# Kernel tuning notes

Hardware: AMD Instinct MI355X
Metric: run time of the kernel (lower is better)

## Reference

```python
import jax, jax.numpy as jnp
import numpy as np

HEADS = 16
DIM_HEAD = 64
EPS = 1e-12  # F.normalize default eps


def setup_inputs() -> dict:
    key = jax.random.key(0)
    k1, k2, k3 = jax.random.split(key, 3)
    b, n, dim = 2, 2048, 1024
    dim_inner = HEADS * DIM_HEAD
    x = jax.random.normal(k1, (b, n, dim), dtype=jnp.float32)
    gamma = jnp.ones((dim,), dtype=jnp.float32)
    w_qkv = jax.random.normal(k2, (dim, 3 * dim_inner), dtype=jnp.float32) * 0.02
    w_out = jax.random.normal(k3, (dim_inner, dim), dtype=jnp.float32) * 0.02
    return {"x": x, "gamma": gamma, "w_qkv": w_qkv, "w_out": w_out}


def reference(x, gamma, w_qkv, w_out):
    b, n, dim = x.shape
    h, d = HEADS, DIM_HEAD
    scale = d ** -0.5

    # RMSNorm (lucidrains): F.normalize(x, dim=-1) * dim**0.5 * gamma
    norm = jnp.sqrt(jnp.sum(x * x, axis=-1, keepdims=True))
    xn = x / jnp.maximum(norm, EPS) * (dim ** 0.5) * gamma

    # qkv projection -> [b, n, 3, h, d] -> q/k/v each [b, h, n, d]
    qkv = (xn @ w_qkv).reshape(b, n, 3, h, d)
    qkv = jnp.transpose(qkv, (2, 0, 3, 1, 4))
    q, k, v = qkv[0], qkv[1], qkv[2]

    q = q * scale
    sim = jnp.einsum('bhid,bhjd->bhij', q, k)  # [b, h, n, n]
    causal_mask = jnp.triu(jnp.ones((n, n), dtype=bool), k=1)
    mask_value = -jnp.finfo(sim.dtype).max
    sim = jnp.where(causal_mask, mask_value, sim)
    attn = jax.nn.softmax(sim, axis=-1)
    out = jnp.einsum('bhij,bhjd->bhid', attn, v)  # [b, h, n, d]

    out = jnp.transpose(out, (0, 2, 1, 3)).reshape(b, n, h * d)
    return out @ w_out
```

## Files before the change

### kernel.cpp

```cpp
#include <hip/hip_runtime.h>

typedef __attribute__((ext_vector_type(8))) short bf16x8;
typedef __attribute__((ext_vector_type(4))) short bf16x4;
typedef __attribute__((ext_vector_type(4))) float f32x4;

static __device__ __forceinline__ short f2bf(float f) {
    union { float f; unsigned u; } v; v.f = f;
    unsigned r = v.u + 0x7fffu + ((v.u >> 16) & 1u);
    return (short)(r >> 16);
}

static __device__ __forceinline__ void async_copy16(const short* g, short* l) {
    __builtin_amdgcn_global_load_lds((const __attribute__((address_space(1))) void*)g,
                                     (__attribute__((address_space(3))) void*)l,
                                     16, 0, 0);
}

#define HEADS 16
#define DHEAD 64
#define NSEQ  2048
#define DIM   1024
#define BATCH 2
#define ROWS  (BATCH * NSEQ)
#define NQKV  (3 * HEADS * DHEAD)

__global__ __launch_bounds__(256) void prep_kernel(const float* __restrict__ x,
                                                   const float* __restrict__ gamma,
                                                   const float* __restrict__ w_qkv,
                                                   const float* __restrict__ w_out,
                                                   short* __restrict__ xn,
                                                   short* __restrict__ wqkvT,
                                                   short* __restrict__ woutT) {
    const int blk = blockIdx.x;
    const int t = threadIdx.x;
    __shared__ float tile[64][65];
    __shared__ float part[4];

    if (blk < 1024) {
        const float* in;  short* out;  int C, bx, by;
        if (blk < 768) { in = w_qkv; out = wqkvT; C = NQKV; bx = blk % 48; by = blk / 48; }
        else           { in = w_out; out = woutT; C = DIM;  bx = (blk - 768) & 15; by = (blk - 768) >> 4; }
        const int gx = bx * 64, gy = by * 64;
        const int lc4 = (t & 15) * 4;
        const int lr  = t >> 4;
#pragma unroll
        for (int p = 0; p < 4; ++p) {
            const float4 v = *(const float4*)&in[(size_t)(gy + p * 16 + lr) * C + gx + lc4];
            tile[p * 16 + lr][lc4 + 0] = v.x;
            tile[p * 16 + lr][lc4 + 1] = v.y;
            tile[p * 16 + lr][lc4 + 2] = v.z;
            tile[p * 16 + lr][lc4 + 3] = v.w;
        }
        __syncthreads();
        const int oc  = t >> 2;
        const int or4 = (t & 3) * 16;
#pragma unroll
        for (int j = 0; j < 4; ++j) {
            bf16x4 w;
#pragma unroll
            for (int r = 0; r < 4; ++r) w[r] = f2bf(tile[or4 + j * 4 + r][oc]);
            *(bf16x4*)&out[(size_t)(gx + oc) * DIM + gy + or4 + j * 4] = w;
        }
    } else {
        const int row = blk - 1024;
        const float4 v = ((const float4*)(x + (size_t)row * DIM))[t];
        float s = v.x * v.x + v.y * v.y + v.z * v.z + v.w * v.w;
#pragma unroll
        for (int off = 32; off > 0; off >>= 1) s += __shfl_down(s, off, 64);
        if ((t & 63) == 0) part[t >> 6] = s;
        __syncthreads();
        const float tot = part[0] + part[1] + part[2] + part[3];
        const float scale = 32.0f / fmaxf(sqrtf(tot), 1e-12f);
        const float4 g = ((const float4*)gamma)[t];
        bf16x4 o;
        o[0] = f2bf(v.x * scale * g.x);
        o[1] = f2bf(v.y * scale * g.y);
        o[2] = f2bf(v.z * scale * g.z);
        o[3] = f2bf(v.w * scale * g.w);
        *(bf16x4*)(xn + (size_t)row * DIM + t * 4) = o;
    }
}

template <int MODE, int MT, int NT, int WM, int WN>
__global__ __launch_bounds__(256) void gemm_bt(const short* __restrict__ A,
                                               const short* __restrict__ Bt,
                                               void* __restrict__ Cout,
                                               short* __restrict__ vtOut,
                                               int K, int N) {
    constexpr int TM = WM * MT * 16;
    constexpr int TN = WN * NT * 16;
    __shared__ alignas(16) short lds_a[2][TM * 32];
    __shared__ alignas(16) short lds_b[2][TN * 32];
    const int tid = threadIdx.x;
    const int lane = tid & 63, wid = tid >> 6;
    const int quad = lane >> 4, l16 = lane & 15;
    const int wm = wid / WN, wn = wid % WN;

    const int nx = gridDim.x;
    const int nwg = nx * gridDim.y;
    int flat = blockIdx.y * nx + blockIdx.x;
    if ((nwg & 7) == 0) {
        const int q8 = nwg >> 3;
        flat = (flat & 7) * q8 + (flat >> 3);
    }
    const int mb = (flat / nx) * TM, nb = (flat % nx) * TN;

    f32x4 acc[MT][NT];
#pragma unroll
    for (int i = 0; i < MT; ++i)
#pragma unroll
        for (int j = 0; j < NT; ++j) acc[i][j] = (f32x4){0.f, 0.f, 0.f, 0.f};

    const int lr = lane >> 2;
    const int lc = (lane & 3) * 8;

    auto stage = [&](int kb, int buf) {
#pragma unroll
        for (int c = 0; c < TM / 64; ++c) {
            const int row = c * 64 + wid * 16 + lr;
            async_copy16(&A[(size_t)(mb + row) * K + kb + lc], &lds_a[buf][row * 32 + lc]);
        }
#pragma unroll
        for (int c = 0; c < TN / 64; ++c) {
            const int row = c * 64 + wid * 16 + lr;
            async_copy16(&Bt[(size_t)(nb + row) * K + kb + lc], &lds_b[buf][row * 32 + lc]);
        }
    };

    stage(0, 0);
    __syncthreads();

    int cur = 0;
    for (int kb = 0; kb < K; kb += 32) {
        if (kb + 32 < K) stage(kb + 32, cur ^ 1);

        bf16x8 af[MT], bfr[NT];
#pragma unroll
        for (int mt = 0; mt < MT; ++mt)
            af[mt] = *(const bf16x8*)&lds_a[cur][(wm * MT * 16 + mt * 16 + l16) * 32 + quad * 8];
#pragma unroll
        for (int nt = 0; nt < NT; ++nt)
            bfr[nt] = *(const bf16x8*)&lds_b[cur][(wn * NT * 16 + nt * 16 + l16) * 32 + quad * 8];
#pragma unroll
        for (int mt = 0; mt < MT; ++mt)
#pragma unroll
            for (int nt = 0; nt < NT; ++nt)
                acc[mt][nt] = __builtin_amdgcn_mfma_f32_16x16x32_bf16(af[mt], bfr[nt],
                                                                      acc[mt][nt], 0, 0, 0);

        __syncthreads();
        cur ^= 1;
    }

#pragma unroll
    for (int mt = 0; mt < MT; ++mt) {
#pragma unroll
        for (int nt = 0; nt < NT; ++nt) {
            const int grow0 = mb + wm * MT * 16 + mt * 16 + quad * 4;
            const int gcol  = nb + wn * NT * 16 + nt * 16 + l16;
            if (MODE == 0) {
                const int s3 = gcol >> 10, rem = gcol & 1023;
                const int hh = rem >> 6, dd = rem & 63;
                const int bb = grow0 >> 11, npos0 = grow0 & 2047;
                if (s3 == 2) {
                    bf16x4 vw;
#pragma unroll
                    for (int r = 0; r < 4; ++r) vw[r] = f2bf(acc[mt][nt][r]);
                    *(bf16x4*)&vtOut[((size_t)(bb * 16 + hh) * 64 + dd) * 2048 + npos0] = vw;
                } else {
                    const float sc = (s3 == 0) ? 0.125f : 1.0f;
#pragma unroll
                    for (int r = 0; r < 4; ++r)
                        ((short*)Cout)[(size_t)((s3 * 32 + bb * 16 + hh) * 2048 + npos0 + r) * 64 +
                                       dd] = f2bf(acc[mt][nt][r] * sc);
                }
            } else {
#pragma unroll
                for (int r = 0; r < 4; ++r)
                    ((float*)Cout)[(size_t)(grow0 + r) * N + gcol] = acc[mt][nt][r];
            }
        }
    }
}

__global__ __launch_bounds__(256, 3) void attn_kernel(const short* __restrict__ qg,
                                                      const short* __restrict__ kg,
                                                      const short* __restrict__ vtg,
                                                      short* __restrict__ og) {
    const int tid = threadIdx.x;
    const int wid = tid >> 6, lane = tid & 63;
    const int quad = lane >> 4, l16 = lane & 15;
    const int blk = blockIdx.x;
    const int qt = (blk < 256) ? (15 - (blk >> 5)) : ((blk - 256) >> 5);
    const int bh = blk & 31;
    const size_t base = (size_t)bh * (NSEQ * DHEAD);
    const int bb = bh >> 4, hh = bh & 15;
    const int qbase = qt * 128 + wid * 32;
    const int ntiles = 2 * qt + 2;

    __shared__ alignas(16) short kA[2][2048], kB[2][2048];
    __shared__ alignas(16) short vA[2][2048], vB[2][2048];

    const int sr = tid >> 2;
    const int sc = (tid & 3) * 8;
    auto stage = [&](int t, short (&KB_)[2][2048], short (&VB_)[2][2048]) {
        const int kb = t * 64;
        async_copy16(&kg[base + (size_t)(kb + sr) * 64 + sc],      &KB_[0][sr * 32 + sc]);
        async_copy16(&kg[base + (size_t)(kb + sr) * 64 + 32 + sc], &KB_[1][sr * 32 + sc]);
        async_copy16(&vtg[base + (size_t)sr * 2048 + kb + sc],      &VB_[0][sr * 32 + sc]);
        async_copy16(&vtg[base + (size_t)sr * 2048 + kb + 32 + sc], &VB_[1][sr * 32 + sc]);
    };

    bf16x8 qf[2][2];
#pragma unroll
    for (int qn = 0; qn < 2; ++qn)
#pragma unroll
        for (int kh = 0; kh < 2; ++kh)
            qf[qn][kh] = *(const bf16x8*)&qg[base + (size_t)(qbase + qn * 16 + l16) * DHEAD +
                                            kh * 32 + quad * 8];

    float li[2] = {0.f, 0.f};
    f32x4 accO[2][4];
#pragma unroll
    for (int qn = 0; qn < 2; ++qn)
#pragma unroll
        for (int nc = 0; nc < 4; ++nc) accO[qn][nc] = (f32x4){0.f, 0.f, 0.f, 0.f};

    auto tile_step = [&](const short (&KB_)[2][2048], const short (&VB_)[2][2048], int t) {
        const int kb = t * 64;
        f32x4 sf[2][4];
#pragma unroll
        for (int m = 0; m < 4; ++m) {
            const bf16x8 kf0 = *(const bf16x8*)&KB_[0][(m * 16 + l16) * 32 + quad * 8];
            const bf16x8 kf1 = *(const bf16x8*)&KB_[1][(m * 16 + l16) * 32 + quad * 8];
#pragma unroll
            for (int qn = 0; qn < 2; ++qn) {
                f32x4 z = (f32x4){0.f, 0.f, 0.f, 0.f};
                z = __builtin_amdgcn_mfma_f32_16x16x32_bf16(kf0, qf[qn][0], z, 0, 0, 0);
                sf[qn][m] = __builtin_amdgcn_mfma_f32_16x16x32_bf16(kf1, qf[qn][1], z, 0, 0, 0);
            }
        }
        if (kb + 64 > qbase) {
#pragma unroll
            for (int qn = 0; qn < 2; ++qn) {
                const int myq = qbase + qn * 16 + l16;
#pragma unroll
                for (int m = 0; m < 4; ++m)
#pragma unroll
                    for (int r = 0; r < 4; ++r)
                        if (kb + m * 16 + quad * 4 + r > myq) sf[qn][m][r] = -3.0e38f;
            }
        }
        unsigned c0[2][4], c1[2][4];
#pragma unroll
        for (int qn = 0; qn < 2; ++qn) {
            float rs = 0.f;
#pragma unroll
            for (int m = 0; m < 4; ++m) {
                const float p0 = __expf(sf[qn][m][0]);
                const float p1 = __expf(sf[qn][m][1]);
                const float p2 = __expf(sf[qn][m][2]);
                const float p3 = __expf(sf[qn][m][3]);
                rs += (p0 + p1) + (p2 + p3);
                asm("v_cvt_pk_bf16_f32 %0, %1, %2" : "=v"(c0[qn][m]) : "v"(p0), "v"(p1));
                asm("v_cvt_pk_bf16_f32 %0, %1, %2" : "=v"(c1[qn][m]) : "v"(p2), "v"(p3));
            }
            li[qn] += rs;
        }
        bf16x8 pf[2][2];
#pragma unroll
        for (int qn = 0; qn < 2; ++qn)
#pragma unroll
            for (int ks = 0; ks < 2; ++ks) {
                unsigned a0 = c0[qn][2 * ks], b0 = c0[qn][2 * ks + 1];
                unsigned a1 = c1[qn][2 * ks], b1 = c1[qn][2 * ks + 1];
                asm("v_permlane32_swap_b32 %0, %1" : "+v"(a0), "+v"(b0));
                asm("v_permlane16_swap_b32 %0, %1" : "+v"(a0), "+v"(b0));
                asm("v_permlane32_swap_b32 %0, %1" : "+v"(a1), "+v"(b1));
                asm("v_permlane16_swap_b32 %0, %1" : "+v"(a1), "+v"(b1));
                union { bf16x8 v; unsigned u[4]; } t8;
                t8.u[0] = a0; t8.u[1] = a1; t8.u[2] = b0; t8.u[3] = b1;
                pf[qn][ks] = t8.v;
            }
#pragma unroll
        for (int nc = 0; nc < 4; ++nc) {
            const bf16x8 vf0 = *(const bf16x8*)&VB_[0][(nc * 16 + l16) * 32 + quad * 8];
            const bf16x8 vf1 = *(const bf16x8*)&VB_[1][(nc * 16 + l16) * 32 + quad * 8];
#pragma unroll
            for (int qn = 0; qn < 2; ++qn) {
                accO[qn][nc] = __builtin_amdgcn_mfma_f32_16x16x32_bf16(vf0, pf[qn][0],
                                                                      accO[qn][nc], 0, 0, 0);
                accO[qn][nc] = __builtin_amdgcn_mfma_f32_16x16x32_bf16(vf1, pf[qn][1],
                                                                      accO[qn][nc], 0, 0, 0);
            }
        }
    };

    stage(0, kA, vA);
    __syncthreads();
    for (int t = 0; t < ntiles; t += 2) {
        stage(t + 1, kB, vB);
        tile_step(kA, vA, t);
        __syncthreads();
        if (t + 2 < ntiles) stage(t + 2, kA, vA);
        tile_step(kB, vB, t + 1);
        __syncthreads();
    }

#pragma unroll
    for (int qn = 0; qn < 2; ++qn) {
        li[qn] += __shfl_xor(li[qn], 16, 64);
        li[qn] += __shfl_xor(li[qn], 32, 64);
        const float inv = 1.0f / li[qn];
        const int npos = qbase + qn * 16 + l16;
#pragma unroll
        for (int nc = 0; nc < 4; ++nc) {
            bf16x4 ow;
#pragma unroll
            for (int r = 0; r < 4; ++r) ow[r] = f2bf(accO[qn][nc][r] * inv);
            *(bf16x4*)&og[(size_t)(bb * 2048 + npos) * 1024 + hh * 64 + nc * 16 + quad * 4] = ow;
        }
    }
}

extern "C" void kernel_launch(void* const* d_in, const int* in_sizes, int n_in,
                              void* d_out, int out_size, void* d_ws, size_t ws_size,
                              hipStream_t stream) {
    const float* x     = (const float*)d_in[0];
    const float* gamma = (const float*)d_in[1];
    const float* w_qkv = (const float*)d_in[2];
    const float* w_out = (const float*)d_in[3];
    float* out = (float*)d_out;
    char* ws = (char*)d_ws;

    short* xn     = (short*)(ws);
    short* wqkvT  = (short*)(ws + 8388608);
    short* woutT  = (short*)(ws + 14680064);
    short* q      = (short*)(ws + 16777216);
    short* k      = q + 32 * 2048 * 64;
    short* vt     = k + 32 * 2048 * 64;
    short* attn   = (short*)(ws + 41943040);

    prep_kernel<<<5120, 256, 0, stream>>>(x, gamma, w_qkv, w_out, xn, wqkvT, woutT);
    gemm_bt<0, 4, 4, 2, 2><<<dim3(NQKV / 128, ROWS / 128), 256, 0, stream>>>(xn, wqkvT, q, vt,
                                                                             DIM, NQKV);
    attn_kernel<<<512, 256, 0, stream>>>(q, k, vt, attn);
    gemm_bt<1, 2, 4, 4, 1><<<dim3(DIM / 64, ROWS / 128), 256, 0, stream>>>(attn, woutT, out,
                                                                           nullptr, DIM, DIM);
}
```

Baseline: 165.9 us.

## Halve attention query tile to 64 rows, double grid, use exp2 with prescaled Q

Each attention block now processes 64 query rows, 16 per wave, instead of 128, and the grid doubles to 1024 blocks. The causal loop handles an odd number of key tiles. Q is prescaled by scale*log2(e) so the softmax can use exp2f, and s_setprio raises wave priority around the MFMA sections. Occupancy is raised to 4 blocks per CU. The intent is better load balance and more waves in flight, at the cost of reloading each K/V tile for more query blocks and halving MFMA work per LDS load.

```diff
diff --git a/kernel.cpp b/kernel.cpp
--- a/kernel.cpp
+++ b/kernel.cpp
@@ -23,6 +23,8 @@
 #define BATCH 2
 #define ROWS  (BATCH * NSEQ)
 #define NQKV  (3 * HEADS * DHEAD)
+
+#define QSCALE 0.18033688f
 
 __global__ __launch_bounds__(256) void prep_kernel(const float* __restrict__ x,
                                                    const float* __restrict__ gamma,
@@ -168,7 +170,7 @@
                     for (int r = 0; r < 4; ++r) vw[r] = f2bf(acc[mt][nt][r]);
                     *(bf16x4*)&vtOut[((size_t)(bb * 16 + hh) * 64 + dd) * 2048 + npos0] = vw;
                 } else {
-                    const float sc = (s3 == 0) ? 0.125f : 1.0f;
+                    const float sc = (s3 == 0) ? QSCALE : 1.0f;
 #pragma unroll
                     for (int r = 0; r < 4; ++r)
                         ((short*)Cout)[(size_t)((s3 * 32 + bb * 16 + hh) * 2048 + npos0 + r) * 64 +
@@ -183,7 +185,7 @@
     }
 }
 
-__global__ __launch_bounds__(256, 3) void attn_kernel(const short* __restrict__ qg,
+__global__ __launch_bounds__(256, 4) void attn_kernel(const short* __restrict__ qg,
                                                       const short* __restrict__ kg,
                                                       const short* __restrict__ vtg,
                                                       short* __restrict__ og) {
@@ -191,12 +193,12 @@
     const int wid = tid >> 6, lane = tid & 63;
     const int quad = lane >> 4, l16 = lane & 15;
     const int blk = blockIdx.x;
-    const int qt = (blk < 256) ? (15 - (blk >> 5)) : ((blk - 256) >> 5);
+    const int qt = (blk < 512) ? (31 - (blk >> 5)) : ((blk - 512) >> 5);
     const int bh = blk & 31;
     const size_t base = (size_t)bh * (NSEQ * DHEAD);
     const int bb = bh >> 4, hh = bh & 15;
-    const int qbase = qt * 128 + wid * 32;
-    const int ntiles = 2 * qt + 2;
+    const int qbase = qt * 64 + wid * 16;
+    const int ntiles = qt + 1;
 
     __shared__ alignas(16) short kA[2][2048], kB[2][2048];
     __shared__ alignas(16) short vA[2][2048], vB[2][2048];
@@ -211,115 +213,97 @@
         async_copy16(&vtg[base + (size_t)sr * 2048 + kb + 32 + sc], &VB_[1][sr * 32 + sc]);
     };
 
-    bf16x8 qf[2][2];
-#pragma unroll
-    for (int qn = 0; qn < 2; ++qn)
-#pragma unroll
-        for (int kh = 0; kh < 2; ++kh)
-            qf[qn][kh] = *(const bf16x8*)&qg[base + (size_t)(qbase + qn * 16 + l16) * DHEAD +
-                                            kh * 32 + quad * 8];
-
-    float li[2] = {0.f, 0.f};
-    f32x4 accO[2][4];
-#pragma unroll
-    for (int qn = 0; qn < 2; ++qn)
-#pragma unroll
-        for (int nc = 0; nc < 4; ++nc) accO[qn][nc] = (f32x4){0.f, 0.f, 0.f, 0.f};
+    bf16x8 qf[2];
+#pragma unroll
+    for (int kh = 0; kh < 2; ++kh)
+        qf[kh] = *(const bf16x8*)&qg[base + (size_t)(qbase + l16) * DHEAD + kh * 32 + quad * 8];
+
+    float li = 0.f;
+    f32x4 accO[4];
+#pragma unroll
+    for (int nc = 0; nc < 4; ++nc) accO[nc] = (f32x4){0.f, 0.f, 0.f, 0.f};
 
     auto tile_step = [&](const short (&KB_)[2][2048], const short (&VB_)[2][2048], int t) {
         const int kb = t * 64;
-        f32x4 sf[2][4];
+        f32x4 sf[4];
+        __builtin_amdgcn_s_setprio(1);
 #pragma unroll
         for (int m = 0; m < 4; ++m) {
             const bf16x8 kf0 = *(const bf16x8*)&KB_[0][(m * 16 + l16) * 32 + quad * 8];
             const bf16x8 kf1 = *(const bf16x8*)&KB_[1][(m * 16 + l16) * 32 + quad * 8];
-#pragma unroll
-            for (int qn = 0; qn < 2; ++qn) {
-                f32x4 z = (f32x4){0.f, 0.f, 0.f, 0.f};
-                z = __builtin_amdgcn_mfma_f32_16x16x32_bf16(kf0, qf[qn][0], z, 0, 0, 0);
-                sf[qn][m] = __builtin_amdgcn_mfma_f32_16x16x32_bf16(kf1, qf[qn][1], z, 0, 0, 0);
-            }
-        }
+            f32x4 z = (f32x4){0.f, 0.f, 0.f, 0.f};
+            z = __builtin_amdgcn_mfma_f32_16x16x32_bf16(kf0, qf[0], z, 0, 0, 0);
+            sf[m] = __builtin_amdgcn_mfma_f32_16x16x32_bf16(kf1, qf[1], z, 0, 0, 0);
+        }
+        __builtin_amdgcn_s_setprio(0);
         if (kb + 64 > qbase) {
-#pragma unroll
-            for (int qn = 0; qn < 2; ++qn) {
-                const int myq = qbase + qn * 16 + l16;
-#pragma unroll
-                for (int m = 0; m < 4; ++m)
-#pragma unroll
-                    for (int r = 0; r < 4; ++r)
-                        if (kb + m * 16 + quad * 4 + r > myq) sf[qn][m][r] = -3.0e38f;
-            }
-        }
-        unsigned c0[2][4], c1[2][4];
-#pragma unroll
-        for (int qn = 0; qn < 2; ++qn) {
-            float rs = 0.f;
-#pragma unroll
-            for (int m = 0; m < 4; ++m) {
-                const float p0 = __expf(sf[qn][m][0]);
-                const float p1 = __expf(sf[qn][m][1]);
-                const float p2 = __expf(sf[qn][m][2]);
-                const float p3 = __expf(sf[qn][m][3]);
-                rs += (p0 + p1) + (p2 + p3);
-                asm("v_cvt_pk_bf16_f32 %0, %1, %2" : "=v"(c0[qn][m]) : "v"(p0), "v"(p1));
-                asm("v_cvt_pk_bf16_f32 %0, %1, %2" : "=v"(c1[qn][m]) : "v"(p2), "v"(p3));
-            }
-            li[qn] += rs;
-        }
-        bf16x8 pf[2][2];
-#pragma unroll
-        for (int qn = 0; qn < 2; ++qn)
-#pragma unroll
-            for (int ks = 0; ks < 2; ++ks) {
-                unsigned a0 = c0[qn][2 * ks], b0 = c0[qn][2 * ks + 1];
-                unsigned a1 = c1[qn][2 * ks], b1 = c1[qn][2 * ks + 1];
-                asm("v_permlane32_swap_b32 %0, %1" : "+v"(a0), "+v"(b0));
-                asm("v_permlane16_swap_b32 %0, %1" : "+v"(a0), "+v"(b0));
-                asm("v_permlane32_swap_b32 %0, %1" : "+v"(a1), "+v"(b1));
-                asm("v_permlane16_swap_b32 %0, %1" : "+v"(a1), "+v"(b1));
-                union { bf16x8 v; unsigned u[4]; } t8;
-                t8.u[0] = a0; t8.u[1] = a1; t8.u[2] = b0; t8.u[3] = b1;
-                pf[qn][ks] = t8.v;
-            }
+            const int myq = qbase + l16;
+#pragma unroll
+            for (int m = 0; m < 4; ++m)
+#pragma unroll
+                for (int r = 0; r < 4; ++r)
+                    if (kb + m * 16 + quad * 4 + r > myq) sf[m][r] = -3.0e38f;
+        }
+        unsigned c0[4], c1[4];
+        float rs = 0.f;
+#pragma unroll
+        for (int m = 0; m < 4; ++m) {
+            const float p0 = exp2f(sf[m][0]);
+            const float p1 = exp2f(sf[m][1]);
+            const float p2 = exp2f(sf[m][2]);
+            const float p3 = exp2f(sf[m][3]);
+            rs += (p0 + p1) + (p2 + p3);
+            asm("v_cvt_pk_bf16_f32 %0, %1, %2" : "=v"(c0[m]) : "v"(p0), "v"(p1));
+            asm("v_cvt_pk_bf16_f32 %0, %1, %2" : "=v"(c1[m]) : "v"(p2), "v"(p3));
+        }
+        li += rs;
+        bf16x8 pf[2];
+#pragma unroll
+        for (int ks = 0; ks < 2; ++ks) {
+            unsigned a0 = c0[2 * ks], b0 = c0[2 * ks + 1];
+            unsigned a1 = c1[2 * ks], b1 = c1[2 * ks + 1];
+            asm("v_permlane32_swap_b32 %0, %1" : "+v"(a0), "+v"(b0));
+            asm("v_permlane16_swap_b32 %0, %1" : "+v"(a0), "+v"(b0));
+            asm("v_permlane32_swap_b32 %0, %1" : "+v"(a1), "+v"(b1));
+            asm("v_permlane16_swap_b32 %0, %1" : "+v"(a1), "+v"(b1));
+            union { bf16x8 v; unsigned u[4]; } t8;
+            t8.u[0] = a0; t8.u[1] = a1; t8.u[2] = b0; t8.u[3] = b1;
+            pf[ks] = t8.v;
+        }
+        __builtin_amdgcn_s_setprio(1);
 #pragma unroll
         for (int nc = 0; nc < 4; ++nc) {
             const bf16x8 vf0 = *(const bf16x8*)&VB_[0][(nc * 16 + l16) * 32 + quad * 8];
             const bf16x8 vf1 = *(const bf16x8*)&VB_[1][(nc * 16 + l16) * 32 + quad * 8];
-#pragma unroll
-            for (int qn = 0; qn < 2; ++qn) {
-                accO[qn][nc] = __builtin_amdgcn_mfma_f32_16x16x32_bf16(vf0, pf[qn][0],
-                                                                      accO[qn][nc], 0, 0, 0);
-                accO[qn][nc] = __builtin_amdgcn_mfma_f32_16x16x32_bf16(vf1, pf[qn][1],
-                                                                      accO[qn][nc], 0, 0, 0);
-            }
-        }
+            accO[nc] = __builtin_amdgcn_mfma_f32_16x16x32_bf16(vf0, pf[0], accO[nc], 0, 0, 0);
+            accO[nc] = __builtin_amdgcn_mfma_f32_16x16x32_bf16(vf1, pf[1], accO[nc], 0, 0, 0);
+        }
+        __builtin_amdgcn_s_setprio(0);
     };
 
     stage(0, kA, vA);
     __syncthreads();
     for (int t = 0; t < ntiles; t += 2) {
-        stage(t + 1, kB, vB);
+        if (t + 1 < ntiles) stage(t + 1, kB, vB);
         tile_step(kA, vA, t);
         __syncthreads();
-        if (t + 2 < ntiles) stage(t + 2, kA, vA);
-        tile_step(kB, vB, t + 1);
-        __syncthreads();
-    }
-
-#pragma unroll
-    for (int qn = 0; qn < 2; ++qn) {
-        li[qn] += __shfl_xor(li[qn], 16, 64);
-        li[qn] += __shfl_xor(li[qn], 32, 64);
-        const float inv = 1.0f / li[qn];
-        const int npos = qbase + qn * 16 + l16;
-#pragma unroll
-        for (int nc = 0; nc < 4; ++nc) {
-            bf16x4 ow;
-#pragma unroll
-            for (int r = 0; r < 4; ++r) ow[r] = f2bf(accO[qn][nc][r] * inv);
-            *(bf16x4*)&og[(size_t)(bb * 2048 + npos) * 1024 + hh * 64 + nc * 16 + quad * 4] = ow;
-        }
+        if (t + 1 < ntiles) {
+            if (t + 2 < ntiles) stage(t + 2, kA, vA);
+            tile_step(kB, vB, t + 1);
+            __syncthreads();
+        }
+    }
+
+    li += __shfl_xor(li, 16, 64);
+    li += __shfl_xor(li, 32, 64);
+    const float inv = 1.0f / li;
+    const int npos = qbase + l16;
+#pragma unroll
+    for (int nc = 0; nc < 4; ++nc) {
+        bf16x4 ow;
+#pragma unroll
+        for (int r = 0; r < 4; ++r) ow[r] = f2bf(accO[nc][r] * inv);
+        *(bf16x4*)&og[(size_t)(bb * 2048 + npos) * 1024 + hh * 64 + nc * 16 + quad * 4] = ow;
     }
 }
 
@@ -344,7 +328,7 @@
     prep_kernel<<<5120, 256, 0, stream>>>(x, gamma, w_qkv, w_out, xn, wqkvT, woutT);
     gemm_bt<0, 4, 4, 2, 2><<<dim3(NQKV / 128, ROWS / 128), 256, 0, stream>>>(xn, wqkvT, q, vt,
                                                                              DIM, NQKV);
-    attn_kernel<<<512, 256, 0, stream>>>(q, k, vt, attn);
+    attn_kernel<<<1024, 256, 0, stream>>>(q, k, vt, attn);
     gemm_bt<1, 2, 4, 4, 1><<<dim3(DIM / 64, ROWS / 128), 256, 0, stream>>>(attn, woutT, out,
                                                                            nullptr, DIM, DIM);
 }
```

After: 169.4 us. 1.02x slower.

## Add dedicated large-tile QKV GEMM with swizzled LDS and split MFMA phases

Applied to the files above, without the earlier changes.

Replaces the generic QKV projection GEMM with a dedicated 512-thread kernel using 256x192 tiles, 64-wide K steps, XOR-swizzled LDS layout, and interleaved LDS reads with MFMA batches under raised wave priority. The Q scale now folds in log2(e) so attention can use exp2f instead of __expf, saving a multiply per element. It also adds s_setprio around the MFMA sections in attention. The larger tile cuts global traffic per FLOP and bank conflicts but raises register and LDS use, limiting occupancy.

```diff
diff --git a/kernel.cpp b/kernel.cpp
--- a/kernel.cpp
+++ b/kernel.cpp
@@ -15,6 +15,13 @@
                                      (__attribute__((address_space(3))) void*)l,
                                      16, 0, 0);
 }
+
+#define BARX()                                            \
+    do {                                                  \
+        asm volatile("" ::: "memory");                    \
+        __builtin_amdgcn_s_barrier();                     \
+        __builtin_amdgcn_sched_barrier(0);                \
+    } while (0)
 
 #define HEADS 16
 #define DHEAD 64
@@ -23,6 +30,8 @@
 #define BATCH 2
 #define ROWS  (BATCH * NSEQ)
 #define NQKV  (3 * HEADS * DHEAD)
+
+#define QSCALE 0.18033688f
 
 __global__ __launch_bounds__(256) void prep_kernel(const float* __restrict__ x,
                                                    const float* __restrict__ gamma,
@@ -81,12 +90,159 @@
     }
 }
 
-template <int MODE, int MT, int NT, int WM, int WN>
-__global__ __launch_bounds__(256) void gemm_bt(const short* __restrict__ A,
-                                               const short* __restrict__ Bt,
-                                               void* __restrict__ Cout,
-                                               short* __restrict__ vtOut,
-                                               int K, int N) {
+__global__ __launch_bounds__(512, 2) void gemm_qkv(const short* __restrict__ A,
+                                                   const short* __restrict__ Bt,
+                                                   short* __restrict__ qkOut,
+                                                   short* __restrict__ vtOut) {
+    __shared__ alignas(16) short lA[2][256 * 64];
+    __shared__ alignas(16) short lB[2][192 * 64];
+    const int tid = threadIdx.x;
+    const int lane = tid & 63, wid = tid >> 6;
+    const int quad = lane >> 4, l16 = lane & 15;
+    const int wm = wid >> 2, wn = wid & 3;
+
+    int flat = blockIdx.x;
+    flat = (flat & 7) * 32 + (flat >> 3);
+    const int mb = (flat >> 4) * 256;
+    const int nb = (flat & 15) * 192;
+
+    f32x4 acc[8][3];
+#pragma unroll
+    for (int i = 0; i < 8; ++i)
+#pragma unroll
+        for (int j = 0; j < 3; ++j) acc[i][j] = (f32x4){0.f, 0.f, 0.f, 0.f};
+
+    const int srow = tid >> 3;
+    const int scol = (tid & 7) * 8;
+    const int scolx = scol ^ ((srow & 7) * 8);
+
+    auto stageA = [&](int kb, int buf) {
+#pragma unroll
+        for (int c = 0; c < 4; ++c) {
+            const int row = c * 64 + srow;
+            async_copy16(&A[(size_t)(mb + row) * 1024 + kb + scolx],
+                         &lA[buf][row * 64 + scol]);
+        }
+    };
+    auto stageB = [&](int kb, int buf) {
+#pragma unroll
+        for (int c = 0; c < 3; ++c) {
+            const int row = c * 64 + srow;
+            async_copy16(&Bt[(size_t)(nb + row) * 1024 + kb + scolx],
+                         &lB[buf][row * 64 + scol]);
+        }
+    };
+    auto rdA = [&](int buf, int mt, int kh) -> bf16x8 {
+        const int row = wm * 128 + mt * 16 + l16;
+        const int col = (kh * 32 + quad * 8) ^ ((row & 7) * 8);
+        return *(const bf16x8*)&lA[buf][row * 64 + col];
+    };
+    auto rdB = [&](int buf, int nt, int kh) -> bf16x8 {
+        const int row = wn * 48 + nt * 16 + l16;
+        const int col = (kh * 32 + quad * 8) ^ ((row & 7) * 8);
+        return *(const bf16x8*)&lB[buf][row * 64 + col];
+    };
+
+    stageA(0, 0);
+    stageB(0, 0);
+    asm volatile("s_waitcnt vmcnt(0)" ::: "memory");
+    BARX();
+
+    int cur = 0;
+    for (int kt = 0; kt < 16; ++kt) {
+        bf16x8 a[4][2], b01[2][2], b2[2];
+#pragma unroll
+        for (int mt = 0; mt < 4; ++mt)
+#pragma unroll
+            for (int kh = 0; kh < 2; ++kh) a[mt][kh] = rdA(cur, mt, kh);
+#pragma unroll
+        for (int nt = 0; nt < 2; ++nt)
+#pragma unroll
+            for (int kh = 0; kh < 2; ++kh) b01[nt][kh] = rdB(cur, nt, kh);
+        if (kt < 15) {
+            stageA((kt + 1) * 64, cur ^ 1);
+            stageB((kt + 1) * 64, cur ^ 1);
+        }
+        BARX();
+        __builtin_amdgcn_s_setprio(1);
+#pragma unroll
+        for (int kh = 0; kh < 2; ++kh)
+#pragma unroll
+            for (int mt = 0; mt < 4; ++mt)
+#pragma unroll
+                for (int nt = 0; nt < 2; ++nt)
+                    acc[mt][nt] = __builtin_amdgcn_mfma_f32_16x16x32_bf16(
+                        a[mt][kh], b01[nt][kh], acc[mt][nt], 0, 0, 0);
+        __builtin_amdgcn_s_setprio(0);
+#pragma unroll
+        for (int kh = 0; kh < 2; ++kh) b2[kh] = rdB(cur, 2, kh);
+        BARX();
+        __builtin_amdgcn_s_setprio(1);
+#pragma unroll
+        for (int kh = 0; kh < 2; ++kh)
+#pragma unroll
+            for (int mt = 0; mt < 4; ++mt)
+                acc[mt][2] = __builtin_amdgcn_mfma_f32_16x16x32_bf16(
+                    a[mt][kh], b2[kh], acc[mt][2], 0, 0, 0);
+        __builtin_amdgcn_s_setprio(0);
+#pragma unroll
+        for (int mt = 0; mt < 4; ++mt)
+#pragma unroll
+            for (int kh = 0; kh < 2; ++kh) a[mt][kh] = rdA(cur, mt + 4, kh);
+        BARX();
+        __builtin_amdgcn_s_setprio(1);
+#pragma unroll
+        for (int kh = 0; kh < 2; ++kh)
+#pragma unroll
+            for (int mt = 0; mt < 4; ++mt)
+                acc[mt + 4][2] = __builtin_amdgcn_mfma_f32_16x16x32_bf16(
+                    a[mt][kh], b2[kh], acc[mt + 4][2], 0, 0, 0);
+        __builtin_amdgcn_s_setprio(0);
+        asm volatile("s_waitcnt vmcnt(0)" ::: "memory");
+        BARX();
+        __builtin_amdgcn_s_setprio(1);
+#pragma unroll
+        for (int kh = 0; kh < 2; ++kh)
+#pragma unroll
+            for (int mt = 0; mt < 4; ++mt)
+#pragma unroll
+                for (int nt = 0; nt < 2; ++nt)
+                    acc[mt + 4][nt] = __builtin_amdgcn_mfma_f32_16x16x32_bf16(
+                        a[mt][kh], b01[nt][kh], acc[mt + 4][nt], 0, 0, 0);
+        __builtin_amdgcn_s_setprio(0);
+        cur ^= 1;
+    }
+
+#pragma unroll
+    for (int mt = 0; mt < 8; ++mt) {
+#pragma unroll
+        for (int nt = 0; nt < 3; ++nt) {
+            const int grow0 = mb + wm * 128 + mt * 16 + quad * 4;
+            const int gcol  = nb + wn * 48 + nt * 16 + l16;
+            const int s3 = gcol >> 10, rem = gcol & 1023;
+            const int hh = rem >> 6, dd = rem & 63;
+            const int bb = grow0 >> 11, npos0 = grow0 & 2047;
+            if (s3 == 2) {
+                bf16x4 vw;
+#pragma unroll
+                for (int r = 0; r < 4; ++r) vw[r] = f2bf(acc[mt][nt][r]);
+                *(bf16x4*)&vtOut[((size_t)(bb * 16 + hh) * 64 + dd) * 2048 + npos0] = vw;
+            } else {
+                const float sc = (s3 == 0) ? QSCALE : 1.0f;
+#pragma unroll
+                for (int r = 0; r < 4; ++r)
+                    qkOut[(size_t)((s3 * 32 + bb * 16 + hh) * 2048 + npos0 + r) * 64 + dd] =
+                        f2bf(acc[mt][nt][r] * sc);
+            }
+        }
+    }
+}
+
+template <int MT, int NT, int WM, int WN>
+__global__ __launch_bounds__(256) void gemm_out(const short* __restrict__ A,
+                                                const short* __restrict__ Bt,
+                                                float* __restrict__ Cout,
+                                                int K, int N) {
     constexpr int TM = WM * MT * 16;
     constexpr int TN = WN * NT * 16;
     __shared__ alignas(16) short lds_a[2][TM * 32];
@@ -147,7 +303,6 @@
             for (int nt = 0; nt < NT; ++nt)
                 acc[mt][nt] = __builtin_amdgcn_mfma_f32_16x16x32_bf16(af[mt], bfr[nt],
                                                                       acc[mt][nt], 0, 0, 0);
-
         __syncthreads();
         cur ^= 1;
     }
@@ -158,27 +313,9 @@
         for (int nt = 0; nt < NT; ++nt) {
             const int grow0 = mb + wm * MT * 16 + mt * 16 + quad * 4;
             const int gcol  = nb + wn * NT * 16 + nt * 16 + l16;
-            if (MODE == 0) {
-                const int s3 = gcol >> 10, rem = gcol & 1023;
-                const int hh = rem >> 6, dd = rem & 63;
-                const int bb = grow0 >> 11, npos0 = grow0 & 2047;
-                if (s3 == 2) {
-                    bf16x4 vw;
-#pragma unroll
-                    for (int r = 0; r < 4; ++r) vw[r] = f2bf(acc[mt][nt][r]);
-                    *(bf16x4*)&vtOut[((size_t)(bb * 16 + hh) * 64 + dd) * 2048 + npos0] = vw;
-                } else {
-                    const float sc = (s3 == 0) ? 0.125f : 1.0f;
-#pragma unroll
-                    for (int r = 0; r < 4; ++r)
-                        ((short*)Cout)[(size_t)((s3 * 32 + bb * 16 + hh) * 2048 + npos0 + r) * 64 +
-                                       dd] = f2bf(acc[mt][nt][r] * sc);
-                }
-            } else {
-#pragma unroll
-                for (int r = 0; r < 4; ++r)
-                    ((float*)Cout)[(size_t)(grow0 + r) * N + gcol] = acc[mt][nt][r];
-            }
+#pragma unroll
+            for (int r = 0; r < 4; ++r)
+                Cout[(size_t)(grow0 + r) * N + gcol] = acc[mt][nt][r];
         }
     }
 }
@@ -229,6 +366,7 @@
     auto tile_step = [&](const short (&KB_)[2][2048], const short (&VB_)[2][2048], int t) {
         const int kb = t * 64;
         f32x4 sf[2][4];
+        __builtin_amdgcn_s_setprio(1);
 #pragma unroll
         for (int m = 0; m < 4; ++m) {
             const bf16x8 kf0 = *(const bf16x8*)&KB_[0][(m * 16 + l16) * 32 + quad * 8];
@@ -240,6 +378,7 @@
                 sf[qn][m] = __builtin_amdgcn_mfma_f32_16x16x32_bf16(kf1, qf[qn][1], z, 0, 0, 0);
             }
         }
+        __builtin_amdgcn_s_setprio(0);
         if (kb + 64 > qbase) {
 #pragma unroll
             for (int qn = 0; qn < 2; ++qn) {
@@ -257,10 +396,10 @@
             float rs = 0.f;
 #pragma unroll
             for (int m = 0; m < 4; ++m) {
-                const float p0 = __expf(sf[qn][m][0]);
-                const float p1 = __expf(sf[qn][m][1]);
-                const float p2 = __expf(sf[qn][m][2]);
-                const float p3 = __expf(sf[qn][m][3]);
+                const float p0 = exp2f(sf[qn][m][0]);
+                const float p1 = exp2f(sf[qn][m][1]);
+                const float p2 = exp2f(sf[qn][m][2]);
+                const float p3 = exp2f(sf[qn][m][3]);
                 rs += (p0 + p1) + (p2 + p3);
                 asm("v_cvt_pk_bf16_f32 %0, %1, %2" : "=v"(c0[qn][m]) : "v"(p0), "v"(p1));
                 asm("v_cvt_pk_bf16_f32 %0, %1, %2" : "=v"(c1[qn][m]) : "v"(p2), "v"(p3));
@@ -282,6 +421,7 @@
                 t8.u[0] = a0; t8.u[1] = a1; t8.u[2] = b0; t8.u[3] = b1;
                 pf[qn][ks] = t8.v;
             }
+        __builtin_amdgcn_s_setprio(1);
 #pragma unroll
         for (int nc = 0; nc < 4; ++nc) {
             const bf16x8 vf0 = *(const bf16x8*)&VB_[0][(nc * 16 + l16) * 32 + quad * 8];
@@ -294,6 +434,7 @@
                                                                       accO[qn][nc], 0, 0, 0);
             }
         }
+        __builtin_amdgcn_s_setprio(0);
     };
 
     stage(0, kA, vA);
@@ -342,9 +483,8 @@
     short* attn   = (short*)(ws + 41943040);
 
     prep_kernel<<<5120, 256, 0, stream>>>(x, gamma, w_qkv, w_out, xn, wqkvT, woutT);
-    gemm_bt<0, 4, 4, 2, 2><<<dim3(NQKV / 128, ROWS / 128), 256, 0, stream>>>(xn, wqkvT, q, vt,
-                                                                             DIM, NQKV);
+    gemm_qkv<<<256, 512, 0, stream>>>(xn, wqkvT, q, vt);
     attn_kernel<<<512, 256, 0, stream>>>(q, k, vt, attn);
-    gemm_bt<1, 2, 4, 4, 1><<<dim3(DIM / 64, ROWS / 128), 256, 0, stream>>>(attn, woutT, out,
-                                                                           nullptr, DIM, DIM);
-}
+    gemm_out<2, 4, 4, 1><<<dim3(DIM / 64, ROWS / 128), 256, 0, stream>>>(attn, woutT, out,
+                                                                         DIM, DIM);
+}
```

New measurement: 173.9 us. 4.8% more time.
